# Optimization experiments

Measured on AMD Instinct MI355X. Metric: run time of the kernel, lower is better.

The kernel has to match this reference:

```python
import jax, jax.numpy as jnp
import numpy as np

V, D, H, L, S = 32000, 1024, 16, 8, 2048
B, T = 2, 1024
HD = D // H


def setup_inputs() -> dict:
    key = jax.random.key(0)
    ks = iter(jax.random.split(key, 16))
    w = lambda shape: jax.random.normal(next(ks), shape, jnp.float32) * 0.02
    return {
        "input_ids": jax.random.randint(next(ks), (B, T), 0, V),
        "text_emb": w((V, D)),
        "pos_emb": w((S, D)),
        "qkv_w": w((L, 3 * D, D)), "qkv_b": jnp.zeros((L, 3 * D)),
        "out_w": w((L, D, D)), "out_b": jnp.zeros((L, D)),
        "ln1_w": jnp.ones((L, D)), "ln1_b": jnp.zeros((L, D)),
        "ln2_w": jnp.ones((L, D)), "ln2_b": jnp.zeros((L, D)),
        "w1": w((L, 4 * D, D)), "b1": jnp.zeros((L, 4 * D)),
        "w2": w((L, D, 4 * D)), "b2": jnp.zeros((L, D)),
        "lnf_w": jnp.ones((D,)), "lnf_b": jnp.zeros((D,)),
        "lm_head_w": w((V, D)),
    }


def layer_norm(x, g, b, eps=1e-5):
    m = jnp.mean(x, -1, keepdims=True)
    v = jnp.var(x, -1, keepdims=True)  # biased var, matches torch LayerNorm
    return (x - m) * jax.lax.rsqrt(v + eps) * g + b


def decoder_block(x, p):
    qkv_w, qkv_b, out_w, out_b, ln1_w, ln1_b, ln2_w, ln2_b, w1, b1, w2, b2 = p
    b_, t_, _ = x.shape
    h = layer_norm(x, ln1_w, ln1_b)
    qkv = h @ qkv_w.T + qkv_b                       # [B,T,3D]
    q, k, v = jnp.split(qkv, 3, axis=-1)
    split = lambda a: a.reshape(b_, t_, H, HD).transpose(0, 2, 1, 3)  # [B,H,T,hd]
    q, k, v = split(q), split(k), split(v)
    scores = jnp.einsum('bhqd,bhkd->bhqk', q, k) * (HD ** -0.5)
    mask = jnp.tril(jnp.ones((t_, t_), bool))
    scores = jnp.where(mask, scores, -jnp.inf)
    attn = jax.nn.softmax(scores, axis=-1)
    o = jnp.einsum('bhqk,bhkd->bhqd', attn, v)
    o = o.transpose(0, 2, 1, 3).reshape(b_, t_, D)
    x = x + o @ out_w.T + out_b
    h = layer_norm(x, ln2_w, ln2_b)
    ff = jax.nn.gelu(h @ w1.T + b1, approximate=False) @ w2.T + b2
    return x + ff


def reference(input_ids, text_emb, pos_emb, qkv_w, qkv_b, out_w, out_b,
              ln1_w, ln1_b, ln2_w, ln2_b, w1, b1, w2, b2,
              lnf_w, lnf_b, lm_head_w):
    t_ = input_ids.shape[1]
    x = text_emb[input_ids] + pos_emb[:t_]          # [B,T,D]
    layer_params = (qkv_w, qkv_b, out_w, out_b, ln1_w, ln1_b,
                    ln2_w, ln2_b, w1, b1, w2, b2)
    def step(x, p):
        return decoder_block(x, p), None
    x, _ = jax.lax.scan(step, x, layer_params)
    x = layer_norm(x, lnf_w, lnf_b)
    logits = x @ lm_head_w.T                        # [B,T,V]
    return logits
```

## Files before the change

kernel.cpp:

```cpp
#include <hip/hip_runtime.h>
#include <hip/hip_bf16.h>

#define Hn 16
#define Dm 1024
#define HDm 64
#define Tn 1024
#define NT 2048
#define Ln 8
#define Vn 32000
#define DFF 4096

typedef unsigned short u16;
typedef unsigned short ushort8 __attribute__((ext_vector_type(8)));
typedef __bf16 bf16x8 __attribute__((ext_vector_type(8)));
typedef float f32x4 __attribute__((ext_vector_type(4)));

__device__ __forceinline__ float b2f(u16 u) {
    union { unsigned int i; float f; } x; x.i = ((unsigned int)u) << 16; return x.f;
}
__device__ __forceinline__ u16 f2b(float f) {
    union { float f; unsigned int i; } x; x.f = f;
    unsigned int r = x.i + 0x7FFFu + ((x.i >> 16) & 1u);
    return (u16)(r >> 16);
}
__device__ __forceinline__ float inload(const void* p, size_t idx, bool isBf) {
    return isBf ? b2f(((const u16*)p)[idx]) : ((const float*)p)[idx];
}

__device__ __forceinline__ void gload16(const void* g, void* l) {
    const unsigned int __attribute__((address_space(1)))* gp =
        (const unsigned int __attribute__((address_space(1)))*)(unsigned long long)g;
    unsigned int __attribute__((address_space(3)))* lp =
        (unsigned int __attribute__((address_space(3)))*)(unsigned int)(unsigned long long)l;
    __builtin_amdgcn_global_load_lds(gp, lp, 16, 0, 0);
}

__global__ __launch_bounds__(256) void sniff_k(const void* temb, int* flag)
{
    int tid = threadIdx.x;
    const u16* p = (const u16*)temb;
    int cnt = 0;
    for (int i = tid; i < 4096; i += 256) {
        float v = b2f(p[2 * i]);
        if (!(fabsf(v) < 8.0f)) cnt++;
    }
    __shared__ int red[256];
    red[tid] = cnt;
    __syncthreads();
    for (int st = 128; st > 0; st >>= 1) {
        if (tid < st) red[tid] += red[tid + st];
        __syncthreads();
    }
    if (tid == 0) flag[0] = (red[0] < 8) ? 1 : 0;
}

__global__ __launch_bounds__(256) void conv_k(
    const void* __restrict__ src, u16* __restrict__ dst, const int* __restrict__ flagp)
{
    if (flagp[0] != 0) return;
    size_t i = ((size_t)blockIdx.x * 256 + threadIdx.x) * 8;
    const float* s = (const float*)src + i;
    f32x4 a = *(const f32x4*)s;
    f32x4 b = *(const f32x4*)(s + 4);
    ushort8 o;
    o[0]=f2b(a[0]); o[1]=f2b(a[1]); o[2]=f2b(a[2]); o[3]=f2b(a[3]);
    o[4]=f2b(b[0]); o[5]=f2b(b[1]); o[6]=f2b(b[2]); o[7]=f2b(b[3]);
    *(ushort8*)(dst + i) = o;
}

__global__ __launch_bounds__(256) void embed_k(
    const int* __restrict__ ids, const void* __restrict__ temb,
    const void* __restrict__ pemb, float* __restrict__ x,
    const int* __restrict__ flagp)
{
    const bool isBf = flagp[0] != 0;
    int n = blockIdx.x;
    int t = n & (Tn - 1);
    int id = ids[n];
    int d = threadIdx.x * 4;
    float* xo = x + (size_t)n * Dm + d;
#pragma unroll
    for (int j = 0; j < 4; ++j)
        xo[j] = inload(temb, (size_t)id * Dm + d + j, isBf)
              + inload(pemb, (size_t)t  * Dm + d + j, isBf);
}

__global__ __launch_bounds__(256) void ln_k(
    const float* __restrict__ x, const void* __restrict__ g,
    const void* __restrict__ bta, size_t goff, u16* __restrict__ hout,
    const int* __restrict__ flagp)
{
    const bool isBf = flagp[0] != 0;
    int n = blockIdx.x;
    int tid = threadIdx.x;
    const float* xr = x + (size_t)n * Dm;
    f32x4 v = *(const f32x4*)&xr[tid * 4];
    float s = v[0] + v[1] + v[2] + v[3];
    float ss = v[0]*v[0] + v[1]*v[1] + v[2]*v[2] + v[3]*v[3];
    __shared__ float r1[256], r2[256];
    r1[tid] = s; r2[tid] = ss;
    __syncthreads();
    for (int st = 128; st > 0; st >>= 1) {
        if (tid < st) { r1[tid] += r1[tid + st]; r2[tid] += r2[tid + st]; }
        __syncthreads();
    }
    float mean = r1[0] * (1.0f / Dm);
    float var  = r2[0] * (1.0f / Dm) - mean * mean;
    float rs = rsqrtf(var + 1e-5f);
    u16* ho = hout + (size_t)n * Dm + tid * 4;
#pragma unroll
    for (int j = 0; j < 4; ++j) {
        float gv = inload(g,   goff + tid * 4 + j, isBf);
        float bv = inload(bta, goff + tid * 4 + j, isBf);
        ho[j] = f2b((v[j] - mean) * rs * gv + bv);
    }
}

__global__ __launch_bounds__(256) void lnfuse_k(
    float* __restrict__ x, const float* __restrict__ P, int nP,
    const void* __restrict__ g, const void* __restrict__ bta, size_t goff,
    u16* __restrict__ hout, const int* __restrict__ flagp)
{
    const bool isBf = flagp[0] != 0;
    int n = blockIdx.x;
    int tid = threadIdx.x;
    float* xr = x + (size_t)n * Dm;
    f32x4 v = *(const f32x4*)&xr[tid * 4];
    if (nP == 2) {
        const float* p0 = P + (size_t)n * Dm;
        const float* p1 = P + (size_t)NT * Dm + (size_t)n * Dm;
        f32x4 a = *(const f32x4*)&p0[tid * 4];
        f32x4 b = *(const f32x4*)&p1[tid * 4];
#pragma unroll
        for (int j = 0; j < 4; ++j) v[j] = v[j] + a[j] + b[j];
        *(f32x4*)&xr[tid * 4] = v;
    }
    float s = v[0] + v[1] + v[2] + v[3];
    float ss = v[0]*v[0] + v[1]*v[1] + v[2]*v[2] + v[3]*v[3];
    __shared__ float r1[256], r2[256];
    r1[tid] = s; r2[tid] = ss;
    __syncthreads();
    for (int st = 128; st > 0; st >>= 1) {
        if (tid < st) { r1[tid] += r1[tid + st]; r2[tid] += r2[tid + st]; }
        __syncthreads();
    }
    float mean = r1[0] * (1.0f / Dm);
    float var  = r2[0] * (1.0f / Dm) - mean * mean;
    float rs = rsqrtf(var + 1e-5f);
    u16* ho = hout + (size_t)n * Dm + tid * 4;
#pragma unroll
    for (int j = 0; j < 4; ++j) {
        float gv = inload(g,   goff + tid * 4 + j, isBf);
        float bv = inload(bta, goff + tid * 4 + j, isBf);
        ho[j] = f2b((v[j] - mean) * rs * gv + bv);
    }
}

template<int EPI>
__global__ __launch_bounds__(256) void gemm_k(
    const u16* __restrict__ A, const void* __restrict__ Bw, size_t woff,
    const void* __restrict__ bias, size_t boff,
    u16* __restrict__ Obf, float* __restrict__ Xres, void* __restrict__ Oext,
    const int* __restrict__ flagp, int M, int N, int K)
{
    const bool isBf = flagp[0] != 0;
    __shared__ __align__(16) u16 As[128][40];
    __shared__ __align__(16) u16 Bs[128][40];
    const int tid  = threadIdx.x;
    const int lane = tid & 63;
    const int wave = tid >> 6;
    const int wr = (wave >> 1) * 64;
    const int wc = (wave & 1) * 64;
    const int row0 = blockIdx.y * 128;
    const int col0 = blockIdx.x * 128;
    const int lr = lane & 15;
    const int lk = (lane >> 4) * 8;
    const int sr = tid >> 2;
    const int sc = (tid & 3) * 8;

    f32x4 acc[4][4] = {};

    for (int k0 = 0; k0 < K; k0 += 32) {
#pragma unroll
        for (int i = 0; i < 2; ++i) {
            int r = sr + i * 64;
            *(ushort8*)&As[r][sc] = *(const ushort8*)&A[(size_t)(row0 + r) * K + k0 + sc];
            size_t be = woff + (size_t)(col0 + r) * K + k0 + sc;
            if (isBf) {
                *(ushort8*)&Bs[r][sc] = *(const ushort8*)&((const u16*)Bw)[be];
            } else {
                const float* src = (const float*)Bw + be;
                f32x4 v0 = *(const f32x4*)src;
                f32x4 v1 = *(const f32x4*)(src + 4);
                ushort8 tv;
                tv[0]=f2b(v0[0]); tv[1]=f2b(v0[1]); tv[2]=f2b(v0[2]); tv[3]=f2b(v0[3]);
                tv[4]=f2b(v1[0]); tv[5]=f2b(v1[1]); tv[6]=f2b(v1[2]); tv[7]=f2b(v1[3]);
                *(ushort8*)&Bs[r][sc] = tv;
            }
        }
        __syncthreads();
        bf16x8 af[4], bfr[4];
#pragma unroll
        for (int m = 0; m < 4; ++m) af[m]  = *(const bf16x8*)&As[wr + m * 16 + lr][lk];
#pragma unroll
        for (int n = 0; n < 4; ++n) bfr[n] = *(const bf16x8*)&Bs[wc + n * 16 + lr][lk];
#pragma unroll
        for (int m = 0; m < 4; ++m)
#pragma unroll
            for (int n = 0; n < 4; ++n)
                acc[m][n] = __builtin_amdgcn_mfma_f32_16x16x32_bf16(af[m], bfr[n], acc[m][n], 0, 0, 0);
        __syncthreads();
    }

    const int rbase = row0 + wr + (lane >> 4) * 4;
    const int cbase = col0 + wc + lr;
#pragma unroll
    for (int n = 0; n < 4; ++n) {
        int c = cbase + n * 16;
        float bv = (bias != nullptr) ? inload(bias, boff + c, isBf) : 0.0f;
#pragma unroll
        for (int m = 0; m < 4; ++m) {
#pragma unroll
            for (int j = 0; j < 4; ++j) {
                int r = rbase + m * 16 + j;
                float v = acc[m][n][j] + bv;
                if (EPI == 1) v = 0.5f * v * (1.0f + erff(v * 0.70710678118f));
                size_t idx = (size_t)r * N + c;
                if (EPI == 2) {
                    Xres[idx] = Xres[idx] + v;
                } else if (EPI == 3) {
                    if (isBf) ((u16*)Oext)[idx] = f2b(v);
                    else      ((float*)Oext)[idx] = v;
                } else {
                    Obf[idx] = f2b(v);
                }
            }
        }
    }
}

template<int EPI>
__global__ __launch_bounds__(256) void gemm2p_k(
    const u16* __restrict__ A, const void* __restrict__ Worig, size_t woff,
    const u16* __restrict__ Wws,
    const void* __restrict__ bias, size_t boff,
    u16* __restrict__ Obf, float* __restrict__ Xres, float* __restrict__ OextA,
    const int* __restrict__ flagp, int N, int Kstride, int Kloop, int nChunk)
{
    const bool isBf = flagp[0] != 0;
    const u16* __restrict__ W = isBf ? ((const u16*)Worig + woff) : Wws;

    __shared__ __align__(16) u16 As[2][128][64];
    __shared__ __align__(16) u16 Bs[2][128][64];

    const int totalT = (N >> 7) * 16;
    const int full = totalT * nChunk;
    const int bid = blockIdx.x;
    const int sidall = (bid & 7) * (full >> 3) + (bid >> 3);
    const int chunk = sidall / totalT;
    const int sid = sidall - chunk * totalT;
    const int row0 = (sid & 15) * 128;
    const int col0 = (sid >> 4) * 128;
    const int kbase = chunk * Kloop;

    const int tid  = threadIdx.x;
    const int lane = tid & 63;
    const int wv   = tid >> 6;
    const int wr = (wv >> 1) * 64;
    const int wc = (wv & 1) * 64;
    const int lr = lane & 15;
    const int lk = (lane >> 4) * 8;
    const int srow8 = lane >> 3;
    const int scol8 = (lane & 7) * 8;

    f32x4 acc[4][4] = {};

    auto STAGE = [&](int bb, int k0) {
#pragma unroll
        for (int i = 0; i < 4; ++i) {
            const int r = wv * 32 + i * 8;
            gload16(&A[(size_t)(row0 + r + srow8) * Kstride + kbase + k0 + scol8], &As[bb][r][0]);
            gload16(&W[(size_t)(col0 + r + srow8) * Kstride + kbase + k0 + scol8], &Bs[bb][r][0]);
        }
    };

    STAGE(0, 0);
    __syncthreads();
    int cur = 0;
    for (int k0 = 0; k0 < Kloop; k0 += 64) {
        if (k0 + 64 < Kloop) STAGE(cur ^ 1, k0 + 64);
#pragma unroll
        for (int kk = 0; kk < 2; ++kk) {
            bf16x8 af[4], bfr[4];
#pragma unroll
            for (int m = 0; m < 4; ++m)
                af[m]  = *(const bf16x8*)&As[cur][wr + m * 16 + lr][kk * 32 + lk];
#pragma unroll
            for (int n = 0; n < 4; ++n)
                bfr[n] = *(const bf16x8*)&Bs[cur][wc + n * 16 + lr][kk * 32 + lk];
#pragma unroll
            for (int m = 0; m < 4; ++m)
#pragma unroll
                for (int n = 0; n < 4; ++n)
                    acc[m][n] = __builtin_amdgcn_mfma_f32_16x16x32_bf16(af[m], bfr[n], acc[m][n], 0, 0, 0);
        }
        __syncthreads();
        cur ^= 1;
    }

    const int rbase = row0 + wr + (lane >> 4) * 4;
    const int cbase = col0 + wc + lr;
#pragma unroll
    for (int n = 0; n < 4; ++n) {
        int c = cbase + n * 16;
        float bv = (bias != nullptr && chunk == 0) ? inload(bias, boff + c, isBf) : 0.0f;
#pragma unroll
        for (int m = 0; m < 4; ++m) {
#pragma unroll
            for (int j = 0; j < 4; ++j) {
                int r = rbase + m * 16 + j;
                float v = acc[m][n][j] + bv;
                if (EPI == 1) v = 0.5f * v * (1.0f + erff(v * 0.70710678118f));
                size_t idx = (size_t)r * N + c;
                if (EPI == 2) {
                    Xres[idx] = Xres[idx] + v;
                } else if (EPI == 4) {
                    OextA[(size_t)chunk * NT * N + idx] = v;
                } else {
                    Obf[idx] = f2b(v);
                }
            }
        }
    }
}

template<int EPI>
__global__ __launch_bounds__(512, 2) void gemm3_k(
    const u16* __restrict__ A, const void* __restrict__ Worig, size_t woff,
    const u16* __restrict__ Wws,
    const void* __restrict__ bias, size_t boff,
    u16* __restrict__ Obf, void* __restrict__ Oext,
    const int* __restrict__ flagp, int N, int K)
{
    const bool isBf = flagp[0] != 0;
    const u16* __restrict__ W = isBf ? ((const u16*)Worig + woff) : Wws;

    __shared__ __align__(16) u16 As[2][256][64];
    __shared__ __align__(16) u16 Bs[2][256][64];

    const int total = (N >> 8) * 8;
    const int bid = blockIdx.x;
    const int sid = (bid & 7) * (total >> 3) + (bid >> 3);
    const int row0 = (sid & 7) * 256;
    const int col0 = (sid >> 3) * 256;

    const int tid  = threadIdx.x;
    const int lane = tid & 63;
    const int wv   = tid >> 6;
    const int wm   = wv >> 2;
    const int wn   = wv & 3;
    const int lr   = lane & 15;
    const int lk   = (lane >> 4) * 8;
    const int grow = lane >> 3;
    const int gcol = (lane & 7) * 8;

    f32x4 acc[8][4] = {};

    auto STAGE = [&](int bb, int k0) {
#pragma unroll
        for (int j = 0; j < 4; ++j) {
            const int r = j * 64 + wv * 8;
            gload16(&A[(size_t)(row0 + r + grow) * K + k0 + gcol], &As[bb][r][0]);
            gload16(&W[(size_t)(col0 + r + grow) * K + k0 + gcol], &Bs[bb][r][0]);
        }
    };

    STAGE(0, 0);
    __syncthreads();
    int cur = 0;
    for (int k0 = 0; k0 < K; k0 += 64) {
        if (k0 + 64 < K) STAGE(cur ^ 1, k0 + 64);
#pragma unroll
        for (int kk = 0; kk < 2; ++kk) {
            bf16x8 af[8], bfr[4];
#pragma unroll
            for (int m = 0; m < 8; ++m)
                af[m] = *(const bf16x8*)&As[cur][wm * 128 + m * 16 + lr][kk * 32 + lk];
#pragma unroll
            for (int n = 0; n < 4; ++n)
                bfr[n] = *(const bf16x8*)&Bs[cur][wn * 64 + n * 16 + lr][kk * 32 + lk];
#pragma unroll
            for (int m = 0; m < 8; ++m)
#pragma unroll
                for (int n = 0; n < 4; ++n)
                    acc[m][n] = __builtin_amdgcn_mfma_f32_16x16x32_bf16(af[m], bfr[n], acc[m][n], 0, 0, 0);
        }
        __syncthreads();
        cur ^= 1;
    }

    const int rbase = row0 + wm * 128 + (lane >> 4) * 4;
    const int cbase = col0 + wn * 64 + lr;
#pragma unroll
    for (int n = 0; n < 4; ++n) {
        int c = cbase + n * 16;
        float bv = (bias != nullptr) ? inload(bias, boff + c, isBf) : 0.0f;
#pragma unroll
        for (int m = 0; m < 8; ++m) {
#pragma unroll
            for (int j = 0; j < 4; ++j) {
                int r = rbase + m * 16 + j;
                float v = acc[m][n][j] + bv;
                size_t idx = (size_t)r * N + c;
                if (EPI == 3) {
                    if (isBf) ((u16*)Oext)[idx] = f2b(v);
                    else      ((float*)Oext)[idx] = v;
                } else {
                    Obf[idx] = f2b(v);
                }
            }
        }
    }
}

__global__ __launch_bounds__(256) void vtrans_k(
    const u16* __restrict__ qkv, u16* __restrict__ vt)
{
    __shared__ __align__(16) u16 til[64][72];
    const int bid = blockIdx.x;
    const int kt = bid & 15;
    const int bh = bid >> 4;
    const int b = bh >> 4, hh = bh & 15;
    const int tid = threadIdx.x;
    const int r = tid >> 2;
    const int c = (tid & 3) * 16;
    const u16* src = qkv + (size_t)(b * Tn + kt * 64 + r) * (3 * Dm) + 2 * Dm + hh * HDm + c;
    *(ushort8*)&til[r][c]     = *(const ushort8*)&src[0];
    *(ushort8*)&til[r][c + 8] = *(const ushort8*)&src[8];
    __syncthreads();
    u16* dst = vt + (size_t)(bh * HDm + r) * Tn + kt * 64 + c;
    ushort8 o1, o2;
#pragma unroll
    for (int j = 0; j < 8; ++j) { o1[j] = til[c + j][r]; o2[j] = til[c + 8 + j][r]; }
    *(ushort8*)&dst[0] = o1;
    *(ushort8*)&dst[8] = o2;
}

__global__ __launch_bounds__(64) void fattn2_k(
    const u16* __restrict__ qkv, const u16* __restrict__ vt, u16* __restrict__ attn)
{
    __shared__ __align__(16) u16 Ps[16][40];

    const int bid = blockIdx.x;
    const int bh  = bid & 31;
    const int qt  = 63 - (bid >> 5);
    const int b = bh >> 4, hh = bh & 15;
    const int lane = threadIdx.x;
    const int lr = lane & 15;
    const int g  = lane >> 4;
    const int lk = g * 8;

    const size_t qbase = (size_t)b * Tn * 3 * Dm + (size_t)hh * HDm;
    const int q0 = qt * 16;

    bf16x8 aq[2];
#pragma unroll
    for (int kh = 0; kh < 2; ++kh)
        aq[kh] = *(const bf16x8*)&qkv[qbase + (size_t)(q0 + lr) * (3 * Dm) + kh * 32 + lk];

    f32x4 o[4] = {};
    float mrun[4], lrun[4];
#pragma unroll
    for (int j = 0; j < 4; ++j) { mrun[j] = -3e38f; lrun[j] = 0.0f; }

    const u16* kp  = qkv + qbase + Dm;
    const u16* vtp = vt + (size_t)(bh * HDm) * Tn;

    const int nkv = (qt >> 1) + 1;
    for (int it = 0; it < nkv; ++it) {
        const int kv0 = it * 32;

        f32x4 s[2] = {};
#pragma unroll
        for (int n = 0; n < 2; ++n)
#pragma unroll
            for (int kh = 0; kh < 2; ++kh) {
                bf16x8 bk = *(const bf16x8*)&kp[(size_t)(kv0 + n * 16 + lr) * (3 * Dm) + kh * 32 + lk];
                s[n] = __builtin_amdgcn_mfma_f32_16x16x32_bf16(aq[kh], bk, s[n], 0, 0, 0);
            }

        float scale[4];
#pragma unroll
        for (int j = 0; j < 4; ++j) {
            const int qrow = q0 + g * 4 + j;
            float v0 = (kv0 + lr      <= qrow) ? s[0][j] * 0.125f : -3e38f;
            float v1 = (kv0 + 16 + lr <= qrow) ? s[1][j] * 0.125f : -3e38f;
            float rm = fmaxf(v0, v1);
#pragma unroll
            for (int msk = 1; msk < 16; msk <<= 1)
                rm = fmaxf(rm, __shfl_xor(rm, msk));
            float mnew = fmaxf(mrun[j], rm);
            scale[j] = __expf(mrun[j] - mnew);
            float p0 = __expf(v0 - mnew);
            float p1 = __expf(v1 - mnew);
            s[0][j] = p0; s[1][j] = p1;
            float rs = p0 + p1;
#pragma unroll
            for (int msk = 1; msk < 16; msk <<= 1)
                rs += __shfl_xor(rs, msk);
            lrun[j] = lrun[j] * scale[j] + rs;
            mrun[j] = mnew;
        }

#pragma unroll
        for (int n = 0; n < 2; ++n)
#pragma unroll
            for (int j = 0; j < 4; ++j)
                Ps[g * 4 + j][n * 16 + lr] = f2b(s[n][j]);
        bf16x8 ap = *(const bf16x8*)&Ps[lr][lk];

#pragma unroll
        for (int d = 0; d < 4; ++d) {
            f32x4 c = o[d];
#pragma unroll
            for (int j = 0; j < 4; ++j) c[j] *= scale[j];
            bf16x8 bv = *(const bf16x8*)&vtp[(size_t)(d * 16 + lr) * Tn + kv0 + lk];
            o[d] = __builtin_amdgcn_mfma_f32_16x16x32_bf16(ap, bv, c, 0, 0, 0);
        }
    }

#pragma unroll
    for (int d = 0; d < 4; ++d)
#pragma unroll
        for (int j = 0; j < 4; ++j) {
            const int qrow = q0 + g * 4 + j;
            attn[(size_t)(b * Tn + qrow) * Dm + hh * HDm + d * 16 + lr] =
                f2b(o[d][j] / lrun[j]);
        }
}

__global__ __launch_bounds__(256) void fattn_k(
    const u16* __restrict__ qkv, u16* __restrict__ attn)
{
    __shared__ __align__(16) u16 Ks[32][72];
    __shared__ __align__(16) u16 Vt[64][40];
    __shared__ __align__(16) u16 Ps[4][16][40];

    const int bid  = blockIdx.x;
    const int pair = bid & 7;
    const int h    = (bid >> 3) & 15;
    const int b    = bid >> 7;
    const int tid  = threadIdx.x;
    const int lane = tid & 63;
    const int wv   = tid >> 6;
    const int lr   = lane & 15;
    const int g    = lane >> 4;
    const int lk   = g * 8;

    const size_t base = (size_t)b * Tn * 3 * Dm + (size_t)h * HDm;
    const int srow = tid >> 3;
    const int sc8  = (tid & 7) * 8;

    for (int half = 0; half < 2; ++half) {
        const int jt = (half == 0) ? pair : 15 - pair;
        const int q0 = jt * 64 + wv * 16;

        bf16x8 aq[2];
#pragma unroll
        for (int kh = 0; kh < 2; ++kh)
            aq[kh] = *(const bf16x8*)&qkv[base + (size_t)(q0 + lr) * (3 * Dm) + kh * 32 + lk];

        f32x4 o[4] = {};
        float mrun[4], lrun[4];
#pragma unroll
        for (int j = 0; j < 4; ++j) { mrun[j] = -3e38f; lrun[j] = 0.0f; }

        const int nkv = 2 * jt + 2;
        for (int it = 0; it < nkv; ++it) {
            const int kv0 = it * 32;
            __syncthreads();
            {
                const size_t rbase = base + (size_t)(kv0 + srow) * (3 * Dm);
                *(ushort8*)&Ks[srow][sc8] = *(const ushort8*)&qkv[rbase + Dm + sc8];
                ushort8 vvv = *(const ushort8*)&qkv[rbase + 2 * Dm + sc8];
#pragma unroll
                for (int jj = 0; jj < 8; ++jj) Vt[sc8 + jj][srow] = vvv[jj];
            }
            __syncthreads();

            f32x4 s[2] = {};
#pragma unroll
            for (int kh = 0; kh < 2; ++kh) {
#pragma unroll
                for (int n = 0; n < 2; ++n) {
                    bf16x8 bk = *(const bf16x8*)&Ks[n * 16 + lr][kh * 32 + lk];
                    s[n] = __builtin_amdgcn_mfma_f32_16x16x32_bf16(aq[kh], bk, s[n], 0, 0, 0);
                }
            }

            float scale[4];
#pragma unroll
            for (int j = 0; j < 4; ++j) {
                const int qrow = q0 + g * 4 + j;
                float v0 = (kv0 + lr      <= qrow) ? s[0][j] * 0.125f : -3e38f;
                float v1 = (kv0 + 16 + lr <= qrow) ? s[1][j] * 0.125f : -3e38f;
                float rm = fmaxf(v0, v1);
#pragma unroll
                for (int msk = 1; msk < 16; msk <<= 1)
                    rm = fmaxf(rm, __shfl_xor(rm, msk));
                float mnew = fmaxf(mrun[j], rm);
                scale[j] = __expf(mrun[j] - mnew);
                float p0 = __expf(v0 - mnew);
                float p1 = __expf(v1 - mnew);
                s[0][j] = p0; s[1][j] = p1;
                float rs = p0 + p1;
#pragma unroll
                for (int msk = 1; msk < 16; msk <<= 1)
                    rs += __shfl_xor(rs, msk);
                lrun[j] = lrun[j] * scale[j] + rs;
                mrun[j] = mnew;
            }

#pragma unroll
            for (int n = 0; n < 2; ++n)
#pragma unroll
                for (int j = 0; j < 4; ++j)
                    Ps[wv][g * 4 + j][n * 16 + lr] = f2b(s[n][j]);
            bf16x8 ap = *(const bf16x8*)&Ps[wv][lr][lk];

#pragma unroll
            for (int d = 0; d < 4; ++d) {
                f32x4 c = o[d];
#pragma unroll
                for (int j = 0; j < 4; ++j) c[j] *= scale[j];
                bf16x8 bv = *(const bf16x8*)&Vt[d * 16 + lr][lk];
                o[d] = __builtin_amdgcn_mfma_f32_16x16x32_bf16(ap, bv, c, 0, 0, 0);
            }
        }

#pragma unroll
        for (int d = 0; d < 4; ++d) {
#pragma unroll
            for (int j = 0; j < 4; ++j) {
                const int qrow = q0 + g * 4 + j;
                attn[(size_t)(b * Tn + qrow) * Dm + h * HDm + d * 16 + lr] =
                    f2b(o[d][j] / lrun[j]);
            }
        }
    }
}

extern "C" void kernel_launch(void* const* d_in, const int* in_sizes, int n_in,
                              void* d_out, int out_size, void* d_ws, size_t ws_size,
                              hipStream_t stream)
{
    const int*  ids       = (const int*)d_in[0];
    const void* text_emb  = d_in[1];
    const void* pos_emb   = d_in[2];
    const void* qkv_w     = d_in[3];
    const void* qkv_b     = d_in[4];
    const void* out_w     = d_in[5];
    const void* out_b     = d_in[6];
    const void* ln1_w     = d_in[7];
    const void* ln1_b     = d_in[8];
    const void* ln2_w     = d_in[9];
    const void* ln2_b     = d_in[10];
    const void* w1        = d_in[11];
    const void* b1        = d_in[12];
    const void* w2        = d_in[13];
    const void* b2        = d_in[14];
    const void* lnf_w     = d_in[15];
    const void* lnf_b     = d_in[16];
    const void* lm_head_w = d_in[17];

    char* ws = (char*)d_ws;
    size_t used = 0;
    auto carve = [&](size_t bytes) { char* p = ws + used; used += (bytes + 15) & ~15ull; return p; };

    int*   flag = (int*)  carve(16);
    float* x    = (float*)carve((size_t)NT * Dm * 4);
    u16*   h    = (u16*)  carve((size_t)NT * Dm * 2);
    u16*   qkv  = (u16*)  carve((size_t)NT * 3 * Dm * 2);
    u16*   attn = (u16*)  carve((size_t)NT * Dm * 2);
    u16*   u    = (u16*)  carve((size_t)NT * DFF * 2);

    u16*   vt = h;
    float* Pf = (float*)qkv;
    float* Pa = (float*)u;

    const size_t nLM  = (size_t)Vn * Dm;
    const size_t nQKV = (size_t)Ln * 3 * Dm * Dm;
    const size_t nOUT = (size_t)Ln * Dm * Dm;
    const size_t nW1  = (size_t)Ln * DFF * Dm;
    const size_t nW2  = (size_t)Ln * Dm * DFF;

    u16* wsLM  = (u16*)carve(nLM * 2);
    size_t lm_used = used;
    u16* wsQKV = (u16*)carve(nQKV * 2);
    u16* wsOUT = (u16*)carve(nOUT * 2);
    u16* wsW1  = (u16*)carve(nW1 * 2);
    u16* wsW2  = (u16*)carve(nW2 * 2);
    size_t t2_used = used;

    const int tier = (ws_size >= t2_used) ? 2 : (ws_size >= lm_used ? 1 : 0);

    dim3 blk(256);

    sniff_k<<<1, blk, 0, stream>>>(text_emb, flag);

    if (tier >= 1)
        conv_k<<<nLM / 2048, blk, 0, stream>>>(lm_head_w, wsLM, flag);
    if (tier >= 2) {
        conv_k<<<nQKV / 2048, blk, 0, stream>>>(qkv_w, wsQKV, flag);
        conv_k<<<nOUT / 2048, blk, 0, stream>>>(out_w, wsOUT, flag);
        conv_k<<<nW1  / 2048, blk, 0, stream>>>(w1,    wsW1,  flag);
        conv_k<<<nW2  / 2048, blk, 0, stream>>>(w2,    wsW2,  flag);
    }

    embed_k<<<NT, blk, 0, stream>>>(ids, text_emb, pos_emb, x, flag);

    if (tier >= 2) {
        for (int l = 0; l < Ln; ++l) {
            size_t oQW = (size_t)l * 3 * Dm * Dm, oQB = (size_t)l * 3 * Dm;
            size_t oOW = (size_t)l * Dm * Dm,     oOB = (size_t)l * Dm;
            size_t oW1 = (size_t)l * DFF * Dm,    oB1 = (size_t)l * DFF;
            size_t oW2 = (size_t)l * Dm * DFF,    oB2 = (size_t)l * Dm;
            size_t oLN = (size_t)l * Dm;

            lnfuse_k<<<NT, blk, 0, stream>>>(x, Pf, (l == 0) ? 0 : 2,
                                             ln1_w, ln1_b, oLN, h, flag);
            gemm2p_k<0><<<16 * (3 * Dm / 128), blk, 0, stream>>>(
                h, qkv_w, oQW, wsQKV + oQW, qkv_b, oQB, qkv, nullptr, nullptr,
                flag, 3 * Dm, Dm, Dm, 1);
            vtrans_k<<<32 * 16, blk, 0, stream>>>(qkv, vt);
            fattn2_k<<<2048, dim3(64), 0, stream>>>(qkv, vt, attn);
            gemm2p_k<4><<<2 * 16 * (Dm / 128), blk, 0, stream>>>(
                attn, out_w, oOW, wsOUT + oOW, out_b, oOB, nullptr, nullptr, Pa,
                flag, Dm, Dm, Dm / 2, 2);
            lnfuse_k<<<NT, blk, 0, stream>>>(x, Pa, 2, ln2_w, ln2_b, oLN, h, flag);
            gemm2p_k<1><<<16 * (DFF / 128), blk, 0, stream>>>(
                h, w1, oW1, wsW1 + oW1, b1, oB1, u, nullptr, nullptr,
                flag, DFF, Dm, Dm, 1);
            gemm2p_k<4><<<2 * 16 * (Dm / 128), blk, 0, stream>>>(
                u, w2, oW2, wsW2 + oW2, b2, oB2, nullptr, nullptr, Pf,
                flag, Dm, DFF, DFF / 2, 2);
        }
        lnfuse_k<<<NT, blk, 0, stream>>>(x, Pf, 2, lnf_w, lnf_b, 0, h, flag);
        gemm3_k<3><<<8 * (Vn / 256), dim3(512), 0, stream>>>(
            h, lm_head_w, 0, wsLM, nullptr, 0, nullptr, d_out, flag, Vn, Dm);
    } else {
        for (int l = 0; l < Ln; ++l) {
            size_t oQW = (size_t)l * 3 * Dm * Dm, oQB = (size_t)l * 3 * Dm;
            size_t oOW = (size_t)l * Dm * Dm,     oOB = (size_t)l * Dm;
            size_t oW1 = (size_t)l * DFF * Dm,    oB1 = (size_t)l * DFF;
            size_t oW2 = (size_t)l * Dm * DFF,    oB2 = (size_t)l * Dm;
            size_t oLN = (size_t)l * Dm;

            ln_k<<<NT, blk, 0, stream>>>(x, ln1_w, ln1_b, oLN, h, flag);
            gemm_k<0><<<dim3(3 * Dm / 128, NT / 128), blk, 0, stream>>>(
                h, qkv_w, oQW, qkv_b, oQB, qkv, nullptr, nullptr, flag, NT, 3 * Dm, Dm);
            fattn_k<<<2 * Hn * 8, blk, 0, stream>>>(qkv, attn);
            gemm_k<2><<<dim3(Dm / 128, NT / 128), blk, 0, stream>>>(
                attn, out_w, oOW, out_b, oOB, nullptr, x, nullptr, flag, NT, Dm, Dm);
            ln_k<<<NT, blk, 0, stream>>>(x, ln2_w, ln2_b, oLN, h, flag);
            gemm_k<1><<<dim3(DFF / 128, NT / 128), blk, 0, stream>>>(
                h, w1, oW1, b1, oB1, u, nullptr, nullptr, flag, NT, DFF, Dm);
            gemm_k<2><<<dim3(Dm / 128, NT / 128), blk, 0, stream>>>(
                u, w2, oW2, b2, oB2, nullptr, x, nullptr, flag, NT, Dm, DFF);
        }
        ln_k<<<NT, blk, 0, stream>>>(x, lnf_w, lnf_b, 0, h, flag);
        if (tier == 1)
            gemm3_k<3><<<8 * (Vn / 256), dim3(512), 0, stream>>>(
                h, lm_head_w, 0, wsLM, nullptr, 0, nullptr, d_out, flag, Vn, Dm);
        else
            gemm_k<3><<<dim3(Vn / 128, NT / 128), blk, 0, stream>>>(
                h, lm_head_w, 0, nullptr, 0, nullptr, nullptr, d_out, flag, NT, Vn, Dm);
    }
}
```

Before: 2.137 ms.

## Restructure LM-head GEMM into 8-wave quadrant pipeline with fine-grained waits

```diff
diff --git a/kernel.cpp b/kernel.cpp
--- a/kernel.cpp
+++ b/kernel.cpp
@@ -335,7 +335,7 @@
 }
 
 template<int EPI>
-__global__ __launch_bounds__(512, 2) void gemm3_k(
+__global__ __launch_bounds__(512, 2) void gemm8_k(
     const u16* __restrict__ A, const void* __restrict__ Worig, size_t woff,
     const u16* __restrict__ Wws,
     const void* __restrict__ bias, size_t boff,
@@ -366,50 +366,84 @@
 
     f32x4 acc[8][4] = {};
 
-    auto STAGE = [&](int bb, int k0) {
-#pragma unroll
-        for (int j = 0; j < 4; ++j) {
-            const int r = j * 64 + wv * 8;
-            gload16(&A[(size_t)(row0 + r + grow) * K + k0 + gcol], &As[bb][r][0]);
-            gload16(&W[(size_t)(col0 + r + grow) * K + k0 + gcol], &Bs[bb][r][0]);
+    auto STAGE_H = [&](int bb, int k0, int h) {
+        const int rb = (h & 1) * 128 + wv * 16;
+#pragma unroll
+        for (int i = 0; i < 2; ++i) {
+            const int r = rb + i * 8;
+            if (h < 2)
+                gload16(&A[(size_t)(row0 + r + grow) * K + k0 + gcol], &As[bb][r][0]);
+            else
+                gload16(&W[(size_t)(col0 + r + grow) * K + k0 + gcol], &Bs[bb][r][0]);
         }
     };
 
-    STAGE(0, 0);
-    __syncthreads();
-    int cur = 0;
-    for (int k0 = 0; k0 < K; k0 += 64) {
-        if (k0 + 64 < K) STAGE(cur ^ 1, k0 + 64);
-#pragma unroll
-        for (int kk = 0; kk < 2; ++kk) {
-            bf16x8 af[8], bfr[4];
-#pragma unroll
-            for (int m = 0; m < 8; ++m)
-                af[m] = *(const bf16x8*)&As[cur][wm * 128 + m * 16 + lr][kk * 32 + lk];
-#pragma unroll
-            for (int n = 0; n < 4; ++n)
-                bfr[n] = *(const bf16x8*)&Bs[cur][wn * 64 + n * 16 + lr][kk * 32 + lk];
-#pragma unroll
-            for (int m = 0; m < 8; ++m)
-#pragma unroll
-                for (int n = 0; n < 4; ++n)
-                    acc[m][n] = __builtin_amdgcn_mfma_f32_16x16x32_bf16(af[m], bfr[n], acc[m][n], 0, 0, 0);
-        }
-        __syncthreads();
-        cur ^= 1;
-    }
-
-    const int rbase = row0 + wm * 128 + (lane >> 4) * 4;
-    const int cbase = col0 + wn * 64 + lr;
+    STAGE_H(0, 0, 0); STAGE_H(0, 0, 2); STAGE_H(0, 0, 3); STAGE_H(0, 0, 1);
+    asm volatile("s_waitcnt vmcnt(0)" ::: "memory");
+    __builtin_amdgcn_s_barrier();
+    asm volatile("" ::: "memory");
+
+    const int nt = K >> 6;
+    for (int t = 0; t < nt; ++t) {
+        const int cur = t & 1;
+        const bool pf = (t + 1 < nt);
+        const int k1 = (t + 1) << 6;
+        bf16x8 af[4][2];
+#pragma unroll
+        for (int p = 0; p < 4; ++p) {
+            const int horder = (p == 0) ? 0 : (p == 1) ? 2 : (p == 2) ? 3 : 1;
+            if (pf) STAGE_H(cur ^ 1, k1, horder);
+            if (p < 3) {
+                if (pf) asm volatile("s_waitcnt vmcnt(6)" ::: "memory");
+                else    asm volatile("s_waitcnt vmcnt(0)" ::: "memory");
+            }
+            asm volatile("" ::: "memory");
+            __builtin_amdgcn_s_barrier();
+            asm volatile("" ::: "memory");
+
+            const int mh = p >> 1, nh = p & 1;
+            if (nh == 0) {
+#pragma unroll
+                for (int m = 0; m < 4; ++m)
+#pragma unroll
+                    for (int kk = 0; kk < 2; ++kk)
+                        af[m][kk] = *(const bf16x8*)&As[cur][mh * 128 + wm * 64 + m * 16 + lr][kk * 32 + lk];
+            }
+            bf16x8 bfr[2][2];
+#pragma unroll
+            for (int n = 0; n < 2; ++n)
+#pragma unroll
+                for (int kk = 0; kk < 2; ++kk)
+                    bfr[n][kk] = *(const bf16x8*)&Bs[cur][nh * 128 + wn * 32 + n * 16 + lr][kk * 32 + lk];
+
+            __builtin_amdgcn_s_setprio(1);
+#pragma unroll
+            for (int m = 0; m < 4; ++m)
+#pragma unroll
+                for (int n = 0; n < 2; ++n)
+#pragma unroll
+                    for (int kk = 0; kk < 2; ++kk)
+                        acc[mh * 4 + m][nh * 2 + n] = __builtin_amdgcn_mfma_f32_16x16x32_bf16(
+                            af[m][kk], bfr[n][kk], acc[mh * 4 + m][nh * 2 + n], 0, 0, 0);
+            __builtin_amdgcn_s_setprio(0);
+            asm volatile("" ::: "memory");
+            __builtin_amdgcn_s_barrier();
+            asm volatile("" ::: "memory");
+        }
+    }
+
 #pragma unroll
     for (int n = 0; n < 4; ++n) {
-        int c = cbase + n * 16;
+        const int nh = n >> 1, nn = n & 1;
+        int c = col0 + nh * 128 + wn * 32 + nn * 16 + lr;
         float bv = (bias != nullptr) ? inload(bias, boff + c, isBf) : 0.0f;
 #pragma unroll
         for (int m = 0; m < 8; ++m) {
+            const int mh = m >> 2, mm = m & 3;
+            const int rb = row0 + mh * 128 + wm * 64 + mm * 16 + (lane >> 4) * 4;
 #pragma unroll
             for (int j = 0; j < 4; ++j) {
-                int r = rbase + m * 16 + j;
+                int r = rb + j;
                 float v = acc[m][n][j] + bv;
                 size_t idx = (size_t)r * N + c;
                 if (EPI == 3) {
@@ -746,7 +780,7 @@
                 flag, Dm, DFF, DFF / 2, 2);
         }
         lnfuse_k<<<NT, blk, 0, stream>>>(x, Pf, 2, lnf_w, lnf_b, 0, h, flag);
-        gemm3_k<3><<<8 * (Vn / 256), dim3(512), 0, stream>>>(
+        gemm8_k<3><<<8 * (Vn / 256), dim3(512), 0, stream>>>(
             h, lm_head_w, 0, wsLM, nullptr, 0, nullptr, d_out, flag, Vn, Dm);
     } else {
         for (int l = 0; l < Ln; ++l) {
@@ -770,7 +804,7 @@
         }
         ln_k<<<NT, blk, 0, stream>>>(x, lnf_w, lnf_b, 0, h, flag);
         if (tier == 1)
-            gemm3_k<3><<<8 * (Vn / 256), dim3(512), 0, stream>>>(
+            gemm8_k<3><<<8 * (Vn / 256), dim3(512), 0, stream>>>(
                 h, lm_head_w, 0, wsLM, nullptr, 0, nullptr, d_out, flag, Vn, Dm);
         else
             gemm_k<3><<<dim3(Vn / 128, NT / 128), blk, 0, stream>>>(
```

Measured after the change: 2.162 ms. Within noise of the previous version (+1.2%).

## Process two query tiles per wave to reuse K/V loads in flash attention

Applied to the files above, without the earlier changes.

```diff
diff --git a/kernel.cpp b/kernel.cpp
--- a/kernel.cpp
+++ b/kernel.cpp
@@ -446,97 +446,121 @@
     *(ushort8*)&dst[8] = o2;
 }
 
-__global__ __launch_bounds__(64) void fattn2_k(
+__global__ __launch_bounds__(256) void fattn3_k(
     const u16* __restrict__ qkv, const u16* __restrict__ vt, u16* __restrict__ attn)
 {
-    __shared__ __align__(16) u16 Ps[16][40];
+    __shared__ __align__(16) u16 Ps[4][2][16][40];
 
     const int bid = blockIdx.x;
     const int bh  = bid & 31;
-    const int qt  = 63 - (bid >> 5);
+    const int qg  = 7 - (bid >> 5);
     const int b = bh >> 4, hh = bh & 15;
-    const int lane = threadIdx.x;
+    const int tid = threadIdx.x;
+    const int wv  = tid >> 6;
+    const int lane = tid & 63;
     const int lr = lane & 15;
     const int g  = lane >> 4;
     const int lk = g * 8;
 
     const size_t qbase = (size_t)b * Tn * 3 * Dm + (size_t)hh * HDm;
-    const int q0 = qt * 16;
-
-    bf16x8 aq[2];
-#pragma unroll
-    for (int kh = 0; kh < 2; ++kh)
-        aq[kh] = *(const bf16x8*)&qkv[qbase + (size_t)(q0 + lr) * (3 * Dm) + kh * 32 + lk];
-
-    f32x4 o[4] = {};
-    float mrun[4], lrun[4];
-#pragma unroll
-    for (int j = 0; j < 4; ++j) { mrun[j] = -3e38f; lrun[j] = 0.0f; }
+    const int q0 = qg * 128 + wv * 32;
+
+    bf16x8 aq[2][2];
+#pragma unroll
+    for (int t = 0; t < 2; ++t)
+#pragma unroll
+        for (int kh = 0; kh < 2; ++kh)
+            aq[t][kh] = *(const bf16x8*)&qkv[qbase + (size_t)(q0 + t * 16 + lr) * (3 * Dm) + kh * 32 + lk];
+
+    f32x4 o[2][4] = {};
+    float mrun[2][4], lrun[2][4];
+#pragma unroll
+    for (int t = 0; t < 2; ++t)
+#pragma unroll
+        for (int j = 0; j < 4; ++j) { mrun[t][j] = -3e38f; lrun[t][j] = 0.0f; }
 
     const u16* kp  = qkv + qbase + Dm;
     const u16* vtp = vt + (size_t)(bh * HDm) * Tn;
 
-    const int nkv = (qt >> 1) + 1;
+    const int nkv = qg * 4 + wv + 1;
     for (int it = 0; it < nkv; ++it) {
         const int kv0 = it * 32;
 
-        f32x4 s[2] = {};
+        bf16x8 bk[2][2];
 #pragma unroll
         for (int n = 0; n < 2; ++n)
 #pragma unroll
-            for (int kh = 0; kh < 2; ++kh) {
-                bf16x8 bk = *(const bf16x8*)&kp[(size_t)(kv0 + n * 16 + lr) * (3 * Dm) + kh * 32 + lk];
-                s[n] = __builtin_amdgcn_mfma_f32_16x16x32_bf16(aq[kh], bk, s[n], 0, 0, 0);
-            }
-
-        float scale[4];
-#pragma unroll
-        for (int j = 0; j < 4; ++j) {
-            const int qrow = q0 + g * 4 + j;
-            float v0 = (kv0 + lr      <= qrow) ? s[0][j] * 0.125f : -3e38f;
-            float v1 = (kv0 + 16 + lr <= qrow) ? s[1][j] * 0.125f : -3e38f;
-            float rm = fmaxf(v0, v1);
-#pragma unroll
-            for (int msk = 1; msk < 16; msk <<= 1)
-                rm = fmaxf(rm, __shfl_xor(rm, msk));
-            float mnew = fmaxf(mrun[j], rm);
-            scale[j] = __expf(mrun[j] - mnew);
-            float p0 = __expf(v0 - mnew);
-            float p1 = __expf(v1 - mnew);
-            s[0][j] = p0; s[1][j] = p1;
-            float rs = p0 + p1;
-#pragma unroll
-            for (int msk = 1; msk < 16; msk <<= 1)
-                rs += __shfl_xor(rs, msk);
-            lrun[j] = lrun[j] * scale[j] + rs;
-            mrun[j] = mnew;
-        }
-
-#pragma unroll
-        for (int n = 0; n < 2; ++n)
-#pragma unroll
-            for (int j = 0; j < 4; ++j)
-                Ps[g * 4 + j][n * 16 + lr] = f2b(s[n][j]);
-        bf16x8 ap = *(const bf16x8*)&Ps[lr][lk];
+            for (int kh = 0; kh < 2; ++kh)
+                bk[n][kh] = *(const bf16x8*)&kp[(size_t)(kv0 + n * 16 + lr) * (3 * Dm) + kh * 32 + lk];
+
+        f32x4 s[2][2] = {};
+#pragma unroll
+        for (int t = 0; t < 2; ++t)
+#pragma unroll
+            for (int n = 0; n < 2; ++n)
+#pragma unroll
+                for (int kh = 0; kh < 2; ++kh)
+                    s[t][n] = __builtin_amdgcn_mfma_f32_16x16x32_bf16(aq[t][kh], bk[n][kh], s[t][n], 0, 0, 0);
+
+        float scale[2][4];
+#pragma unroll
+        for (int t = 0; t < 2; ++t)
+#pragma unroll
+            for (int j = 0; j < 4; ++j) {
+                const int qrow = q0 + t * 16 + g * 4 + j;
+                float v0 = (kv0 + lr      <= qrow) ? s[t][0][j] * 0.125f : -3e38f;
+                float v1 = (kv0 + 16 + lr <= qrow) ? s[t][1][j] * 0.125f : -3e38f;
+                float rm = fmaxf(v0, v1);
+#pragma unroll
+                for (int msk = 1; msk < 16; msk <<= 1)
+                    rm = fmaxf(rm, __shfl_xor(rm, msk));
+                float mnew = fmaxf(mrun[t][j], rm);
+                scale[t][j] = __expf(mrun[t][j] - mnew);
+                float p0 = __expf(v0 - mnew);
+                float p1 = __expf(v1 - mnew);
+                s[t][0][j] = p0; s[t][1][j] = p1;
+                float rs = p0 + p1;
+#pragma unroll
+                for (int msk = 1; msk < 16; msk <<= 1)
+                    rs += __shfl_xor(rs, msk);
+                lrun[t][j] = lrun[t][j] * scale[t][j] + rs;
+                mrun[t][j] = mnew;
+            }
+
+#pragma unroll
+        for (int t = 0; t < 2; ++t)
+#pragma unroll
+            for (int n = 0; n < 2; ++n)
+#pragma unroll
+                for (int j = 0; j < 4; ++j)
+                    Ps[wv][t][g * 4 + j][n * 16 + lr] = f2b(s[t][n][j]);
+        bf16x8 ap[2];
+        ap[0] = *(const bf16x8*)&Ps[wv][0][lr][lk];
+        ap[1] = *(const bf16x8*)&Ps[wv][1][lr][lk];
 
 #pragma unroll
         for (int d = 0; d < 4; ++d) {
-            f32x4 c = o[d];
-#pragma unroll
-            for (int j = 0; j < 4; ++j) c[j] *= scale[j];
             bf16x8 bv = *(const bf16x8*)&vtp[(size_t)(d * 16 + lr) * Tn + kv0 + lk];
-            o[d] = __builtin_amdgcn_mfma_f32_16x16x32_bf16(ap, bv, c, 0, 0, 0);
-        }
-    }
-
-#pragma unroll
-    for (int d = 0; d < 4; ++d)
-#pragma unroll
-        for (int j = 0; j < 4; ++j) {
-            const int qrow = q0 + g * 4 + j;
-            attn[(size_t)(b * Tn + qrow) * Dm + hh * HDm + d * 16 + lr] =
-                f2b(o[d][j] / lrun[j]);
-        }
+#pragma unroll
+            for (int t = 0; t < 2; ++t) {
+                f32x4 c = o[t][d];
+#pragma unroll
+                for (int j = 0; j < 4; ++j) c[j] *= scale[t][j];
+                o[t][d] = __builtin_amdgcn_mfma_f32_16x16x32_bf16(ap[t], bv, c, 0, 0, 0);
+            }
+        }
+    }
+
+#pragma unroll
+    for (int t = 0; t < 2; ++t)
+#pragma unroll
+        for (int d = 0; d < 4; ++d)
+#pragma unroll
+            for (int j = 0; j < 4; ++j) {
+                const int qrow = q0 + t * 16 + g * 4 + j;
+                attn[(size_t)(b * Tn + qrow) * Dm + hh * HDm + d * 16 + lr] =
+                    f2b(o[t][d][j] / lrun[t][j]);
+            }
 }
 
 __global__ __launch_bounds__(256) void fattn_k(
@@ -733,7 +757,7 @@
                 h, qkv_w, oQW, wsQKV + oQW, qkv_b, oQB, qkv, nullptr, nullptr,
                 flag, 3 * Dm, Dm, Dm, 1);
             vtrans_k<<<32 * 16, blk, 0, stream>>>(qkv, vt);
-            fattn2_k<<<2048, dim3(64), 0, stream>>>(qkv, vt, attn);
+            fattn3_k<<<256, blk, 0, stream>>>(qkv, vt, attn);
             gemm2p_k<4><<<2 * 16 * (Dm / 128), blk, 0, stream>>>(
                 attn, out_w, oOW, wsOUT + oOW, out_b, oOB, nullptr, nullptr, Pa,
                 flag, Dm, Dm, Dm / 2, 2);
```

Result: slower. 2.437 ms (+14.0%).
